# Kernel optimization log

Hardware: AMD Instinct MI355X
Metric: run time of the kernel (lower is better)

## Reference

```python
import jax, jax.numpy as jnp
import numpy as np

T, B, I = 2048, 256, 64
H = 1280          # hidden_size = 20 * input_size
H4 = H // 4       # fc2 out / LSTMCell input = 320
H8 = H // 8       # LSTMCell hidden = 160
O = 32            # output_size


def setup_inputs() -> dict:
    key = jax.random.key(0)
    ks = jax.random.split(key, 12)
    n = lambda k, shape, fan: jax.random.normal(k, shape, jnp.float32) * (1.0 / np.sqrt(fan))
    return {
        "inputs": jax.random.normal(ks[0], (T, B, I), jnp.float32),
        "W1": n(ks[1], (H, I), I),
        "b1": jnp.zeros((H,), jnp.float32),
        "W2": n(ks[2], (H4, H), H),
        "b2": jnp.zeros((H4,), jnp.float32),
        "W_ih": n(ks[3], (4 * H8, H4), H4),
        "W_hh": n(ks[4], (4 * H8, H8), H8),
        "b_ih": jnp.zeros((4 * H8,), jnp.float32),
        "b_hh": jnp.zeros((4 * H8,), jnp.float32),
        "W3": n(ks[5], (O, H8), H8),
        "b3": jnp.zeros((O,), jnp.float32),
    }


def reference(inputs, W1, b1, W2, b2, W_ih, W_hh, b_ih, b_hh, W3, b3):
    # Eval-mode forward: dropout / noise are identity when not training.
    Bd = inputs.shape[1]
    Hc = W_hh.shape[1]

    def step(carry, x_t):
        h, c = carry
        x = jax.nn.leaky_relu(x_t @ W1.T + b1)          # [B, H]
        x = jax.nn.leaky_relu(x @ W2.T + b2)            # [B, H//4]
        gates = x @ W_ih.T + b_ih + h @ W_hh.T + b_hh   # [B, 4*H//8]
        i, f, g, o = jnp.split(gates, 4, axis=-1)       # PyTorch gate order i,f,g,o
        i = jax.nn.sigmoid(i)
        f = jax.nn.sigmoid(f)
        g = jnp.tanh(g)
        o = jax.nn.sigmoid(o)
        c = f * c + i * g
        h = o * jnp.tanh(c)
        y = h @ W3.T + b3                                # [B, O]
        return (h, c), y

    h0 = jnp.zeros((Bd, Hc), inputs.dtype)
    c0 = jnp.zeros((Bd, Hc), inputs.dtype)
    _, ys = jax.lax.scan(step, (h0, c0), inputs)         # [T, B, O]
    return ys
```

## Files before the change

### kernel.cpp

```cpp
#include <hip/hip_runtime.h>
#include <hip/hip_bf16.h>

#define T_STEPS 2048
#define BATCH   256
#define INW     64
#define H1      1280
#define H4D     320
#define H8D     160
#define G4      640
#define ONUM    32

typedef __attribute__((ext_vector_type(8))) short short8;
typedef __attribute__((ext_vector_type(4))) float floatx4;
typedef __hip_bfloat16 bf16;

__device__ __forceinline__ float b2f(bf16 v) { return __bfloat162float(v); }
__device__ __forceinline__ bf16  f2b(float v) { return __float2bfloat16(v); }
__device__ __forceinline__ float bfu(unsigned short u) { return __uint_as_float((unsigned)u << 16); }
__device__ __forceinline__ float fsig(float x)  { return __fdividef(1.0f, 1.0f + __expf(-x)); }
__device__ __forceinline__ float ftanh(float x) { return __fdividef(2.0f, 1.0f + __expf(-2.0f * x)) - 1.0f; }

__device__ __forceinline__ void lds_barrier() {
  asm volatile("s_waitcnt lgkmcnt(0)\n\ts_barrier" ::: "memory");
}

struct bf16x4 { bf16 a, b, c, d; };
__global__ void cast_f32_bf16_v4(const float* __restrict__ s, bf16* __restrict__ d, int n4) {
  int i = blockIdx.x * blockDim.x + threadIdx.x;
  if (i >= n4) return;
  float4 v = reinterpret_cast<const float4*>(s)[i];
  bf16x4 o{f2b(v.x), f2b(v.y), f2b(v.z), f2b(v.w)};
  reinterpret_cast<bf16x4*>(d)[i] = o;
}

#define SMEM_BYTES 41472

__device__ void gemm_tile(char* smem, int tid, int mt, int nt,
                          const bf16* __restrict__ A, const bf16* __restrict__ W,
                          const float* __restrict__ bias, const float* __restrict__ bias2,
                          bf16* __restrict__ C, int N, int K, int ACT)
{
  bf16 (*As)[72] = reinterpret_cast<bf16 (*)[72]>(smem);
  bf16 (*Ws)[72] = reinterpret_cast<bf16 (*)[72]>(smem + 128 * 72 * 2);
  const int lane = tid & 63;
  const int wave = tid >> 6;
  const int mrow = lane & 15;
  const int quad = lane >> 4;
  const int wm = (wave >= 5) ? 64 : 0;
  const int wn = (wave - (wave >= 5 ? 5 : 0)) * 32;
  const int bm = mt * 128;
  const int bn = nt * 160;

  floatx4 acc[4][2] = {};

  const int va0 = tid, va1 = tid + 640;
  const int vw0 = tid, vw1 = tid + 640;

  for (int k0 = 0; k0 < K; k0 += 64) {
    short8 a0, a1, w0, w1;
    a0 = *reinterpret_cast<const short8*>(&A[(size_t)(bm + (va0 >> 3)) * K + k0 + (va0 & 7) * 8]);
    if (va1 < 1024)
      a1 = *reinterpret_cast<const short8*>(&A[(size_t)(bm + (va1 >> 3)) * K + k0 + (va1 & 7) * 8]);
    w0 = *reinterpret_cast<const short8*>(&W[(size_t)(bn + (vw0 >> 3)) * K + k0 + (vw0 & 7) * 8]);
    w1 = *reinterpret_cast<const short8*>(&W[(size_t)(bn + (vw1 >> 3)) * K + k0 + (vw1 & 7) * 8]);
    __syncthreads();
    *reinterpret_cast<short8*>(&As[va0 >> 3][(va0 & 7) * 8]) = a0;
    if (va1 < 1024)
      *reinterpret_cast<short8*>(&As[va1 >> 3][(va1 & 7) * 8]) = a1;
    *reinterpret_cast<short8*>(&Ws[vw0 >> 3][(vw0 & 7) * 8]) = w0;
    *reinterpret_cast<short8*>(&Ws[vw1 >> 3][(vw1 & 7) * 8]) = w1;
    __syncthreads();
#pragma unroll
    for (int kk = 0; kk < 2; ++kk) {
      short8 af[4], wf[2];
#pragma unroll
      for (int i = 0; i < 4; ++i)
        af[i] = *reinterpret_cast<const short8*>(&As[wm + i * 16 + mrow][kk * 32 + quad * 8]);
#pragma unroll
      for (int j = 0; j < 2; ++j)
        wf[j] = *reinterpret_cast<const short8*>(&Ws[wn + j * 16 + mrow][kk * 32 + quad * 8]);
#pragma unroll
      for (int i = 0; i < 4; ++i)
#pragma unroll
        for (int j = 0; j < 2; ++j)
          acc[i][j] = __builtin_amdgcn_mfma_f32_16x16x32_bf16(af[i], wf[j], acc[i][j], 0, 0, 0);
    }
  }

#pragma unroll
  for (int j = 0; j < 2; ++j) {
    int col = bn + wn + j * 16 + mrow;
    float bv = (ACT == 2) ? (bias[col] + bias2[col]) : bias[col];
    int g = 0, ix = 0;
    if (ACT == 2) { g = col / 160; ix = col - g * 160; }
#pragma unroll
    for (int i = 0; i < 4; ++i) {
#pragma unroll
      for (int r = 0; r < 4; ++r) {
        int row = bm + wm + i * 16 + quad * 4 + r;
        float v = acc[i][j][r] + bv;
        if (ACT == 1) {
          v = (v > 0.0f) ? v : 0.01f * v;
          C[(size_t)row * N + col] = f2b(v);
        } else {
          C[(size_t)row * 640 + ix * 4 + g] = f2b(v);
        }
      }
    }
  }
}

__device__ void recur_path(char* smem, int tid, int bid,
    const bf16* __restrict__ gx, const bf16* __restrict__ Whh,
    const bf16* __restrict__ W3w, const float* __restrict__ b3,
    bf16* __restrict__ h_ws, float* __restrict__ c_ws,
    float* __restrict__ outp, int Tc, int init)
{
  bf16 (*hbuf)[16][168] = reinterpret_cast<bf16 (*)[16][168]>(smem);
  bf16 (*w3s)[168] = reinterpret_cast<bf16 (*)[168]>(smem + 10752);
  const int lane = tid & 63;
  const int wave = tid >> 6;
  const int mrow = lane & 15;
  const int quad = lane >> 4;
  const int bbase = bid * 4;
  const int ixg = wave * 16 + mrow;

  short8 whf[4][5];
#pragma unroll
  for (int g = 0; g < 4; ++g)
#pragma unroll
    for (int ks = 0; ks < 5; ++ks)
      whf[g][ks] = *reinterpret_cast<const short8*>(
          &Whh[(size_t)(g * 160 + ixg) * 160 + ks * 32 + quad * 8]);

  for (int e = tid; e < 32 * 160; e += 640) {
    int r = e / 160, cix = e - r * 160;
    w3s[r][cix] = W3w[e];
  }
  const float b3v = (wave < 2) ? b3[wave * 16 + mrow] : 0.0f;

  for (int e = tid; e < 2 * 16 * 168; e += 640)
    reinterpret_cast<bf16*>(hbuf)[e] = f2b(0.0f);
  __syncthreads();
  {
    int r = tid / 160, cix = tid - r * 160;
    hbuf[0][r * 4][cix] = init ? f2b(0.0f) : h_ws[(size_t)(bbase + r) * 160 + cix];
  }
  float c0 = init ? 0.0f : c_ws[(size_t)(bbase + quad) * 160 + ixg];
  __syncthreads();

  const uint2* __restrict__ gxp = reinterpret_cast<const uint2*>(gx);
  const size_t goff = (size_t)(bbase + quad) * 160 + ixg;
  uint2 gcur = gxp[goff], gnext = gcur;

  for (int t = 0; t < Tc; ++t) {
    const int rb = t & 1, wb = rb ^ 1;
    if (t + 1 < Tc) gnext = gxp[(size_t)(t + 1) * (256 * 160) + goff];

    short8 af[5];
#pragma unroll
    for (int ks = 0; ks < 5; ++ks)
      af[ks] = *reinterpret_cast<const short8*>(&hbuf[rb][mrow][ks * 32 + quad * 8]);

    if (wave < 2 && t > 0) {
      short8 w3f[5];
#pragma unroll
      for (int ks = 0; ks < 5; ++ks)
        w3f[ks] = *reinterpret_cast<const short8*>(&w3s[wave * 16 + mrow][ks * 32 + quad * 8]);
      floatx4 ya = {};
#pragma unroll
      for (int ks = 0; ks < 5; ++ks)
        ya = __builtin_amdgcn_mfma_f32_16x16x32_bf16(af[ks], w3f[ks], ya, 0, 0, 0);
      outp[((size_t)(t - 1) * 256 + bbase + quad) * 32 + wave * 16 + mrow] = ya[0] + b3v;
    }

    floatx4 acc[4] = {};
#pragma unroll
    for (int ks = 0; ks < 5; ++ks)
#pragma unroll
      for (int g = 0; g < 4; ++g)
        acc[g] = __builtin_amdgcn_mfma_f32_16x16x32_bf16(af[ks], whf[g][ks], acc[g], 0, 0, 0);

    {
      union { uint2 u; unsigned short s[4]; } q;
      q.u = gcur;
      float xi = acc[0][0] + bfu(q.s[0]);
      float xf = acc[1][0] + bfu(q.s[1]);
      float xg = acc[2][0] + bfu(q.s[2]);
      float xo = acc[3][0] + bfu(q.s[3]);
      float iv = fsig(xi), fv = fsig(xf), gvv = ftanh(xg), ov = fsig(xo);
      c0 = fv * c0 + iv * gvv;
      hbuf[wb][quad * 4][ixg] = f2b(ov * ftanh(c0));
    }
    gcur = gnext;
    lds_barrier();
  }

  if (wave < 2) {
    const int rb = Tc & 1;
    short8 af[5], w3f[5];
#pragma unroll
    for (int ks = 0; ks < 5; ++ks) {
      af[ks]  = *reinterpret_cast<const short8*>(&hbuf[rb][mrow][ks * 32 + quad * 8]);
      w3f[ks] = *reinterpret_cast<const short8*>(&w3s[wave * 16 + mrow][ks * 32 + quad * 8]);
    }
    floatx4 ya = {};
#pragma unroll
    for (int ks = 0; ks < 5; ++ks)
      ya = __builtin_amdgcn_mfma_f32_16x16x32_bf16(af[ks], w3f[ks], ya, 0, 0, 0);
    outp[((size_t)(Tc - 1) * 256 + bbase + quad) * 32 + wave * 16 + mrow] = ya[0] + b3v;
  }

  {
    int r = tid / 160, cix = tid - r * 160;
    h_ws[(size_t)(bbase + r) * 160 + cix] = hbuf[Tc & 1][r * 4][cix];
  }
  c_ws[(size_t)(bbase + quad) * 160 + ixg] = c0;
}

__global__ __launch_bounds__(640, 1) void fused_step(
    int has_recur, const bf16* gxr, const bf16* Whh, const bf16* W3w,
    const float* b3, bf16* h_ws, float* c_ws, float* outp, int Tc, int init,
    int nb1, const bf16* A1, const bf16* W1w, const float* b1v, bf16* C1,
    int nb2, const bf16* A2, const bf16* W2w, const float* b2v, bf16* C2,
    int nb3, const bf16* A3, const bf16* Wiw, const float* bihv, const float* bhhv, bf16* C3,
    int nM)
{
  __shared__ __align__(16) char smem[SMEM_BYTES];
  const int tid = threadIdx.x;
  if (blockIdx.x < 64) {
    if (has_recur)
      recur_path(smem, tid, blockIdx.x, gxr, Whh, W3w, b3, h_ws, c_ws, outp, Tc, init);
    return;
  }
  int gb = blockIdx.x - 64;
  if (gb < nb1) {
    gemm_tile(smem, tid, gb % nM, gb / nM, A1, W1w, b1v, nullptr, C1, H1, INW, 1);
    return;
  }
  gb -= nb1;
  if (gb < nb2) {
    gemm_tile(smem, tid, gb % nM, gb / nM, A2, W2w, b2v, nullptr, C2, H4D, H1, 1);
    return;
  }
  gb -= nb2;
  gemm_tile(smem, tid, gb % nM, gb / nM, A3, Wiw, bihv, bhhv, C3, G4, H4D, 2);
}

extern "C" void kernel_launch(void* const* d_in, const int* in_sizes, int n_in,
                              void* d_out, int out_size, void* d_ws, size_t ws_size,
                              hipStream_t stream)
{
  const float* inp = (const float*)d_in[0];
  const float* W1  = (const float*)d_in[1];
  const float* b1  = (const float*)d_in[2];
  const float* W2  = (const float*)d_in[3];
  const float* b2  = (const float*)d_in[4];
  const float* Wih = (const float*)d_in[5];
  const float* Whh = (const float*)d_in[6];
  const float* bih = (const float*)d_in[7];
  const float* bhh = (const float*)d_in[8];
  const float* W3  = (const float*)d_in[9];
  const float* b3  = (const float*)d_in[10];
  float* out = (float*)d_out;

  char* ws = (char*)d_ws;
  size_t off = 0;
  auto alloc = [&](size_t bytes) -> char* {
    char* p = ws + off;
    off += (bytes + 255) & ~(size_t)255;
    return p;
  };

  bf16* inpb = (bf16*)alloc((size_t)T_STEPS * BATCH * INW * 2);
  bf16* w1b  = (bf16*)alloc((size_t)H1 * INW * 2);
  bf16* w2b  = (bf16*)alloc((size_t)H4D * H1 * 2);
  bf16* wihb = (bf16*)alloc((size_t)G4 * H4D * 2);
  bf16* whhb = (bf16*)alloc((size_t)G4 * H8D * 2);
  bf16* w3b  = (bf16*)alloc((size_t)ONUM * H8D * 2);
  bf16* h_ws = (bf16*)alloc((size_t)BATCH * H8D * 2);
  float* c_ws = (float*)alloc((size_t)BATCH * H8D * 4);
  size_t fixed = off;

  int Tc = 128;
  while (Tc > 16) {
    size_t Mc = (size_t)Tc * BATCH;
    size_t need = fixed
      + 2 * ((Mc * H1 * 2 + 255) & ~(size_t)255)
      + 2 * ((Mc * H4D * 2 + 255) & ~(size_t)255)
      + 2 * ((Mc * G4 * 2 + 255) & ~(size_t)255);
    if (need <= ws_size) break;
    Tc >>= 1;
  }
  const size_t Mc = (size_t)Tc * BATCH;
  bf16* x2b[2], *x4b[2], *gxb[2];
  for (int i = 0; i < 2; ++i) x2b[i] = (bf16*)alloc(Mc * H1 * 2);
  for (int i = 0; i < 2; ++i) x4b[i] = (bf16*)alloc(Mc * H4D * 2);
  for (int i = 0; i < 2; ++i) gxb[i] = (bf16*)alloc(Mc * G4 * 2);

  {
    int n4 = T_STEPS * BATCH * INW / 4;
    cast_f32_bf16_v4<<<(n4 + 255) / 256, 256, 0, stream>>>(inp, inpb, n4);
    n4 = H1 * INW / 4;
    cast_f32_bf16_v4<<<(n4 + 255) / 256, 256, 0, stream>>>(W1, w1b, n4);
    n4 = H4D * H1 / 4;
    cast_f32_bf16_v4<<<(n4 + 255) / 256, 256, 0, stream>>>(W2, w2b, n4);
    n4 = G4 * H4D / 4;
    cast_f32_bf16_v4<<<(n4 + 255) / 256, 256, 0, stream>>>(Wih, wihb, n4);
    n4 = G4 * H8D / 4;
    cast_f32_bf16_v4<<<(n4 + 255) / 256, 256, 0, stream>>>(Whh, whhb, n4);
    n4 = ONUM * H8D / 4;
    cast_f32_bf16_v4<<<(n4 + 255) / 256, 256, 0, stream>>>(W3, w3b, n4);
  }

  const int nch = T_STEPS / Tc;
  const int nM = (int)(Mc / 128);

  for (int L = 0; L < nch + 3; ++L) {
    const int cr = L - 3, c1 = L, c2 = L - 1, c3 = L - 2;
    const int nb1 = (c1 >= 0 && c1 < nch) ? nM * (H1 / 160) : 0;
    const int nb2 = (c2 >= 0 && c2 < nch) ? nM * (H4D / 160) : 0;
    const int nb3 = (c3 >= 0 && c3 < nch) ? nM * (G4 / 160) : 0;
    const int hasr = (cr >= 0 && cr < nch) ? 1 : 0;

    const bf16* gxr = gxb[hasr ? (cr & 1) : 0];
    float* outp = hasr ? (out + (size_t)cr * Tc * BATCH * ONUM) : out;
    const bf16* A1 = nb1 ? (inpb + (size_t)c1 * Mc * INW) : inpb;
    bf16* C1 = x2b[nb1 ? (c1 & 1) : 0];
    const bf16* A2 = x2b[nb2 ? (c2 & 1) : 0];
    bf16* C2 = x4b[nb2 ? (c2 & 1) : 0];
    const bf16* A3 = x4b[nb3 ? (c3 & 1) : 0];
    bf16* C3 = gxb[nb3 ? (c3 & 1) : 0];

    fused_step<<<64 + nb1 + nb2 + nb3, 640, 0, stream>>>(
        hasr, gxr, whhb, w3b, b3, h_ws, c_ws, outp, Tc, (cr == 0) ? 1 : 0,
        nb1, A1, w1b, b1, C1,
        nb2, A2, w2b, b2, C2,
        nb3, A3, wihb, bih, bhh, C3,
        nM);
  }
}
```

Before: 2.973 ms.

## Fuse fc1, fc2 and LSTM input projection into one per-tile GEMM chain

```diff
diff --git a/kernel.cpp b/kernel.cpp
--- a/kernel.cpp
+++ b/kernel.cpp
@@ -14,6 +14,8 @@
 typedef __attribute__((ext_vector_type(4))) float floatx4;
 typedef __hip_bfloat16 bf16;
 
+union frag8 { short8 v; uint2 u2[2]; };
+
 __device__ __forceinline__ float b2f(bf16 v) { return __bfloat162float(v); }
 __device__ __forceinline__ bf16  f2b(float v) { return __float2bfloat16(v); }
 __device__ __forceinline__ float bfu(unsigned short u) { return __uint_as_float((unsigned)u << 16); }
@@ -33,78 +35,203 @@
   reinterpret_cast<bf16x4*>(d)[i] = o;
 }
 
-#define SMEM_BYTES 41472
-
-__device__ void gemm_tile(char* smem, int tid, int mt, int nt,
-                          const bf16* __restrict__ A, const bf16* __restrict__ W,
-                          const float* __restrict__ bias, const float* __restrict__ bias2,
-                          bf16* __restrict__ C, int N, int K, int ACT)
+__global__ void cast_permute_wih(const float* __restrict__ s, bf16* __restrict__ d) {
+  int i = blockIdx.x * blockDim.x + threadIdx.x;
+  if (i >= G4 * (H4D / 4)) return;
+  int p = i / (H4D / 4), k4 = (i - p * (H4D / 4)) * 4;
+  int g = p & 3, ix = p >> 2;
+  float4 v = *reinterpret_cast<const float4*>(&s[(size_t)(g * 160 + ix) * H4D + k4]);
+  bf16x4 o{f2b(v.x), f2b(v.y), f2b(v.z), f2b(v.w)};
+  *reinterpret_cast<bf16x4*>(&d[(size_t)p * H4D + k4]) = o;
+}
+
+#define SMEM_BYTES 65024
+
+__device__ void fused_gemm(char* smem, int tid, int gb,
+    const bf16* __restrict__ Xg, const bf16* __restrict__ W1g, const float* __restrict__ b1v,
+    const bf16* __restrict__ W2g, const float* __restrict__ b2v,
+    const bf16* __restrict__ Wpg, const float* __restrict__ bihv, const float* __restrict__ bhhv,
+    bf16* __restrict__ gxw)
 {
-  bf16 (*As)[72] = reinterpret_cast<bf16 (*)[72]>(smem);
-  bf16 (*Ws)[72] = reinterpret_cast<bf16 (*)[72]>(smem + 128 * 72 * 2);
-  const int lane = tid & 63;
-  const int wave = tid >> 6;
-  const int mrow = lane & 15;
-  const int quad = lane >> 4;
-  const int wm = (wave >= 5) ? 64 : 0;
-  const int wn = (wave - (wave >= 5 ? 5 : 0)) * 32;
-  const int bm = mt * 128;
-  const int bn = nt * 160;
-
-  floatx4 acc[4][2] = {};
-
-  const int va0 = tid, va1 = tid + 640;
-  const int vw0 = tid, vw1 = tid + 640;
-
-  for (int k0 = 0; k0 < K; k0 += 64) {
-    short8 a0, a1, w0, w1;
-    a0 = *reinterpret_cast<const short8*>(&A[(size_t)(bm + (va0 >> 3)) * K + k0 + (va0 & 7) * 8]);
-    if (va1 < 1024)
-      a1 = *reinterpret_cast<const short8*>(&A[(size_t)(bm + (va1 >> 3)) * K + k0 + (va1 & 7) * 8]);
-    w0 = *reinterpret_cast<const short8*>(&W[(size_t)(bn + (vw0 >> 3)) * K + k0 + (vw0 & 7) * 8]);
-    w1 = *reinterpret_cast<const short8*>(&W[(size_t)(bn + (vw1 >> 3)) * K + k0 + (vw1 & 7) * 8]);
-    __syncthreads();
-    *reinterpret_cast<short8*>(&As[va0 >> 3][(va0 & 7) * 8]) = a0;
-    if (va1 < 1024)
-      *reinterpret_cast<short8*>(&As[va1 >> 3][(va1 & 7) * 8]) = a1;
-    *reinterpret_cast<short8*>(&Ws[vw0 >> 3][(vw0 & 7) * 8]) = w0;
-    *reinterpret_cast<short8*>(&Ws[vw1 >> 3][(vw1 & 7) * 8]) = w1;
-    __syncthreads();
+  bf16 (*Y1s)[72]  = reinterpret_cast<bf16 (*)[72]>(smem);
+  bf16 (*W2cs)[72] = reinterpret_cast<bf16 (*)[72]>(smem + 9216);
+  const int lane = tid & 63, wave = tid >> 6;
+  const int mrow = lane & 15, quad = lane >> 4;
+  const int wm = (wave >= 5) ? 1 : 0;
+  const int wn = wave - wm * 5;
+  const int fm = wave & 3;
+  const int fnp = (wave >> 2) & 1;
+  const size_t R0 = (size_t)gb * 64;
+
+  short8 xf0, xf1;
+  if (wave < 8) {
+    const bf16* xrow = Xg + (R0 + fm * 16 + mrow) * INW;
+    xf0 = *reinterpret_cast<const short8*>(xrow + quad * 8);
+    xf1 = *reinterpret_cast<const short8*>(xrow + 32 + quad * 8);
+  }
+
+  short8 w2r[4];
+#pragma unroll
+  for (int i = 0; i < 4; ++i) {
+    int v = tid + i * 640;
+    w2r[i] = *reinterpret_cast<const short8*>(&W2g[(size_t)(v >> 3) * H1 + (v & 7) * 8]);
+  }
+#pragma unroll
+  for (int i = 0; i < 4; ++i) {
+    int v = tid + i * 640;
+    *reinterpret_cast<short8*>(&W2cs[v >> 3][(v & 7) * 8]) = w2r[i];
+  }
+
+  floatx4 acc2[2][4] = {};
+
+  for (int c = 0; c < 20; ++c) {
+    if (wave < 8) {
+      const bf16* wr0 = W1g + (size_t)(c * 64 + (fnp * 2 + 0) * 16 + mrow) * INW;
+      const bf16* wr1 = W1g + (size_t)(c * 64 + (fnp * 2 + 1) * 16 + mrow) * INW;
+      short8 wf00 = *reinterpret_cast<const short8*>(wr0 + quad * 8);
+      short8 wf01 = *reinterpret_cast<const short8*>(wr0 + 32 + quad * 8);
+      short8 wf10 = *reinterpret_cast<const short8*>(wr1 + quad * 8);
+      short8 wf11 = *reinterpret_cast<const short8*>(wr1 + 32 + quad * 8);
+      floatx4 a10 = {}, a11 = {};
+      a10 = __builtin_amdgcn_mfma_f32_16x16x32_bf16(xf0, wf00, a10, 0, 0, 0);
+      a10 = __builtin_amdgcn_mfma_f32_16x16x32_bf16(xf1, wf01, a10, 0, 0, 0);
+      a11 = __builtin_amdgcn_mfma_f32_16x16x32_bf16(xf0, wf10, a11, 0, 0, 0);
+      a11 = __builtin_amdgcn_mfma_f32_16x16x32_bf16(xf1, wf11, a11, 0, 0, 0);
+#pragma unroll
+      for (int r = 0; r < 4; ++r) {
+        int row = fm * 16 + quad * 4 + r;
+        {
+          int col = (fnp * 2 + 0) * 16 + mrow;
+          float vv = a10[r] + b1v[c * 64 + col];
+          Y1s[row][col] = f2b(vv > 0.0f ? vv : 0.01f * vv);
+        }
+        {
+          int col = (fnp * 2 + 1) * 16 + mrow;
+          float vv = a11[r] + b1v[c * 64 + col];
+          Y1s[row][col] = f2b(vv > 0.0f ? vv : 0.01f * vv);
+        }
+      }
+    }
+    if (c < 19) {
+#pragma unroll
+      for (int i = 0; i < 4; ++i) {
+        int v = tid + i * 640;
+        w2r[i] = *reinterpret_cast<const short8*>(
+            &W2g[(size_t)(v >> 3) * H1 + (c + 1) * 64 + (v & 7) * 8]);
+      }
+    }
+    lds_barrier();
 #pragma unroll
     for (int kk = 0; kk < 2; ++kk) {
-      short8 af[4], wf[2];
-#pragma unroll
-      for (int i = 0; i < 4; ++i)
-        af[i] = *reinterpret_cast<const short8*>(&As[wm + i * 16 + mrow][kk * 32 + quad * 8]);
-#pragma unroll
-      for (int j = 0; j < 2; ++j)
-        wf[j] = *reinterpret_cast<const short8*>(&Ws[wn + j * 16 + mrow][kk * 32 + quad * 8]);
-#pragma unroll
-      for (int i = 0; i < 4; ++i)
-#pragma unroll
-        for (int j = 0; j < 2; ++j)
-          acc[i][j] = __builtin_amdgcn_mfma_f32_16x16x32_bf16(af[i], wf[j], acc[i][j], 0, 0, 0);
-    }
-  }
-
-#pragma unroll
-  for (int j = 0; j < 2; ++j) {
-    int col = bn + wn + j * 16 + mrow;
-    float bv = (ACT == 2) ? (bias[col] + bias2[col]) : bias[col];
-    int g = 0, ix = 0;
-    if (ACT == 2) { g = col / 160; ix = col - g * 160; }
-#pragma unroll
-    for (int i = 0; i < 4; ++i) {
+      short8 af0 = *reinterpret_cast<const short8*>(&Y1s[wm * 32 + mrow][kk * 32 + quad * 8]);
+      short8 af1 = *reinterpret_cast<const short8*>(&Y1s[wm * 32 + 16 + mrow][kk * 32 + quad * 8]);
+#pragma unroll
+      for (int j = 0; j < 4; ++j) {
+        short8 bfj = *reinterpret_cast<const short8*>(
+            &W2cs[wn * 64 + j * 16 + mrow][kk * 32 + quad * 8]);
+        acc2[0][j] = __builtin_amdgcn_mfma_f32_16x16x32_bf16(af0, bfj, acc2[0][j], 0, 0, 0);
+        acc2[1][j] = __builtin_amdgcn_mfma_f32_16x16x32_bf16(af1, bfj, acc2[1][j], 0, 0, 0);
+      }
+    }
+    lds_barrier();
+    if (c < 19) {
+#pragma unroll
+      for (int i = 0; i < 4; ++i) {
+        int v = tid + i * 640;
+        *reinterpret_cast<short8*>(&W2cs[v >> 3][(v & 7) * 8]) = w2r[i];
+      }
+    }
+  }
+
+  bf16 (*Y2s)[328] = reinterpret_cast<bf16 (*)[328]>(smem);
+  char* Wps = smem + 41984;
+  short8 wpr[2];
+#pragma unroll
+  for (int i = 0; i < 2; ++i) {
+    int v = tid + i * 640;
+    wpr[i] = *reinterpret_cast<const short8*>(&Wpg[(size_t)(v >> 2) * H4D + (v & 3) * 8]);
+  }
+#pragma unroll
+  for (int i = 0; i < 2; ++i) {
+#pragma unroll
+    for (int j = 0; j < 4; ++j) {
+      int col = wn * 64 + j * 16 + mrow;
+      float bb = b2v[col];
 #pragma unroll
       for (int r = 0; r < 4; ++r) {
-        int row = bm + wm + i * 16 + quad * 4 + r;
-        float v = acc[i][j][r] + bv;
-        if (ACT == 1) {
-          v = (v > 0.0f) ? v : 0.01f * v;
-          C[(size_t)row * N + col] = f2b(v);
-        } else {
-          C[(size_t)row * 640 + ix * 4 + g] = f2b(v);
-        }
+        int row = wm * 32 + i * 16 + quad * 4 + r;
+        float vv = acc2[i][j][r] + bb;
+        Y2s[row][col] = f2b(vv > 0.0f ? vv : 0.01f * vv);
+      }
+    }
+  }
+#pragma unroll
+  for (int i = 0; i < 2; ++i) {
+    int v = tid + i * 640;
+    frag8 u; u.v = wpr[i];
+    char* p = Wps + (size_t)(v >> 2) * 72 + (v & 3) * 16;
+    *reinterpret_cast<uint2*>(p) = u.u2[0];
+    *reinterpret_cast<uint2*>(p + 8) = u.u2[1];
+  }
+  lds_barrier();
+
+  floatx4 ag[2][4];
+  for (int t = 0; t < 20; ++t) {
+    int h = t / 10, kc = t - h * 10;
+    if (kc == 0) {
+#pragma unroll
+      for (int i = 0; i < 2; ++i)
+#pragma unroll
+        for (int j = 0; j < 4; ++j) ag[i][j] = (floatx4){0.f, 0.f, 0.f, 0.f};
+    }
+    short8 af0 = *reinterpret_cast<const short8*>(&Y2s[wm * 32 + mrow][kc * 32 + quad * 8]);
+    short8 af1 = *reinterpret_cast<const short8*>(&Y2s[wm * 32 + 16 + mrow][kc * 32 + quad * 8]);
+    frag8 bfj[4];
+#pragma unroll
+    for (int j = 0; j < 4; ++j) {
+      const char* p = Wps + (size_t)(wn * 64 + j * 16 + mrow) * 72 + quad * 16;
+      bfj[j].u2[0] = *reinterpret_cast<const uint2*>(p);
+      bfj[j].u2[1] = *reinterpret_cast<const uint2*>(p + 8);
+    }
+#pragma unroll
+    for (int j = 0; j < 4; ++j) {
+      ag[0][j] = __builtin_amdgcn_mfma_f32_16x16x32_bf16(af0, bfj[j].v, ag[0][j], 0, 0, 0);
+      ag[1][j] = __builtin_amdgcn_mfma_f32_16x16x32_bf16(af1, bfj[j].v, ag[1][j], 0, 0, 0);
+    }
+    if (t < 19) {
+      int nh = (t + 1) / 10, nk = (t + 1) - nh * 10;
+#pragma unroll
+      for (int i = 0; i < 2; ++i) {
+        int v = tid + i * 640;
+        wpr[i] = *reinterpret_cast<const short8*>(
+            &Wpg[(size_t)(nh * 320 + (v >> 2)) * H4D + nk * 32 + (v & 3) * 8]);
+      }
+    }
+    lds_barrier();
+    if (t < 19) {
+#pragma unroll
+      for (int i = 0; i < 2; ++i) {
+        int v = tid + i * 640;
+        frag8 u; u.v = wpr[i];
+        char* p = Wps + (size_t)(v >> 2) * 72 + (v & 3) * 16;
+        *reinterpret_cast<uint2*>(p) = u.u2[0];
+        *reinterpret_cast<uint2*>(p + 8) = u.u2[1];
+      }
+    }
+    lds_barrier();
+    if (kc == 9) {
+#pragma unroll
+      for (int j = 0; j < 4; ++j) {
+        int p = h * 320 + wn * 64 + j * 16 + mrow;
+        int g = p & 3, ix = p >> 2;
+        float bb = bihv[g * 160 + ix] + bhhv[g * 160 + ix];
+#pragma unroll
+        for (int i = 0; i < 2; ++i)
+#pragma unroll
+          for (int r = 0; r < 4; ++r) {
+            int row = wm * 32 + i * 16 + quad * 4 + r;
+            gxw[(R0 + row) * 640 + p] = f2b(ag[i][j][r] + bb);
+          }
       }
     }
   }
@@ -218,13 +345,12 @@
   c_ws[(size_t)(bbase + quad) * 160 + ixg] = c0;
 }
 
-__global__ __launch_bounds__(640, 1) void fused_step(
+__global__ __launch_bounds__(640, 5) void fused_step(
     int has_recur, const bf16* gxr, const bf16* Whh, const bf16* W3w,
     const float* b3, bf16* h_ws, float* c_ws, float* outp, int Tc, int init,
-    int nb1, const bf16* A1, const bf16* W1w, const float* b1v, bf16* C1,
-    int nb2, const bf16* A2, const bf16* W2w, const float* b2v, bf16* C2,
-    int nb3, const bf16* A3, const bf16* Wiw, const float* bihv, const float* bhhv, bf16* C3,
-    int nM)
+    int has_gemm, const bf16* Xc, const bf16* W1w, const float* b1v,
+    const bf16* W2w, const float* b2v, const bf16* Wpw,
+    const float* bihv, const float* bhhv, bf16* gxw)
 {
   __shared__ __align__(16) char smem[SMEM_BYTES];
   const int tid = threadIdx.x;
@@ -233,18 +359,8 @@
       recur_path(smem, tid, blockIdx.x, gxr, Whh, W3w, b3, h_ws, c_ws, outp, Tc, init);
     return;
   }
-  int gb = blockIdx.x - 64;
-  if (gb < nb1) {
-    gemm_tile(smem, tid, gb % nM, gb / nM, A1, W1w, b1v, nullptr, C1, H1, INW, 1);
-    return;
-  }
-  gb -= nb1;
-  if (gb < nb2) {
-    gemm_tile(smem, tid, gb % nM, gb / nM, A2, W2w, b2v, nullptr, C2, H4D, H1, 1);
-    return;
-  }
-  gb -= nb2;
-  gemm_tile(smem, tid, gb % nM, gb / nM, A3, Wiw, bihv, bhhv, C3, G4, H4D, 2);
+  if (has_gemm)
+    fused_gemm(smem, tid, blockIdx.x - 64, Xc, W1w, b1v, W2w, b2v, Wpw, bihv, bhhv, gxw);
 }
 
 extern "C" void kernel_launch(void* const* d_in, const int* in_sizes, int n_in,
@@ -275,7 +391,7 @@
   bf16* inpb = (bf16*)alloc((size_t)T_STEPS * BATCH * INW * 2);
   bf16* w1b  = (bf16*)alloc((size_t)H1 * INW * 2);
   bf16* w2b  = (bf16*)alloc((size_t)H4D * H1 * 2);
-  bf16* wihb = (bf16*)alloc((size_t)G4 * H4D * 2);
+  bf16* wpb  = (bf16*)alloc((size_t)G4 * H4D * 2);
   bf16* whhb = (bf16*)alloc((size_t)G4 * H8D * 2);
   bf16* w3b  = (bf16*)alloc((size_t)ONUM * H8D * 2);
   bf16* h_ws = (bf16*)alloc((size_t)BATCH * H8D * 2);
@@ -285,17 +401,12 @@
   int Tc = 128;
   while (Tc > 16) {
     size_t Mc = (size_t)Tc * BATCH;
-    size_t need = fixed
-      + 2 * ((Mc * H1 * 2 + 255) & ~(size_t)255)
-      + 2 * ((Mc * H4D * 2 + 255) & ~(size_t)255)
-      + 2 * ((Mc * G4 * 2 + 255) & ~(size_t)255);
+    size_t need = fixed + 2 * ((Mc * G4 * 2 + 255) & ~(size_t)255);
     if (need <= ws_size) break;
     Tc >>= 1;
   }
   const size_t Mc = (size_t)Tc * BATCH;
-  bf16* x2b[2], *x4b[2], *gxb[2];
-  for (int i = 0; i < 2; ++i) x2b[i] = (bf16*)alloc(Mc * H1 * 2);
-  for (int i = 0; i < 2; ++i) x4b[i] = (bf16*)alloc(Mc * H4D * 2);
+  bf16* gxb[2];
   for (int i = 0; i < 2; ++i) gxb[i] = (bf16*)alloc(Mc * G4 * 2);
 
   {
@@ -305,8 +416,8 @@
     cast_f32_bf16_v4<<<(n4 + 255) / 256, 256, 0, stream>>>(W1, w1b, n4);
     n4 = H4D * H1 / 4;
     cast_f32_bf16_v4<<<(n4 + 255) / 256, 256, 0, stream>>>(W2, w2b, n4);
-    n4 = G4 * H4D / 4;
-    cast_f32_bf16_v4<<<(n4 + 255) / 256, 256, 0, stream>>>(Wih, wihb, n4);
+    int np = G4 * (H4D / 4);
+    cast_permute_wih<<<(np + 255) / 256, 256, 0, stream>>>(Wih, wpb);
     n4 = G4 * H8D / 4;
     cast_f32_bf16_v4<<<(n4 + 255) / 256, 256, 0, stream>>>(Whh, whhb, n4);
     n4 = ONUM * H8D / 4;
@@ -314,29 +425,18 @@
   }
 
   const int nch = T_STEPS / Tc;
-  const int nM = (int)(Mc / 128);
-
-  for (int L = 0; L < nch + 3; ++L) {
-    const int cr = L - 3, c1 = L, c2 = L - 1, c3 = L - 2;
-    const int nb1 = (c1 >= 0 && c1 < nch) ? nM * (H1 / 160) : 0;
-    const int nb2 = (c2 >= 0 && c2 < nch) ? nM * (H4D / 160) : 0;
-    const int nb3 = (c3 >= 0 && c3 < nch) ? nM * (G4 / 160) : 0;
-    const int hasr = (cr >= 0 && cr < nch) ? 1 : 0;
-
-    const bf16* gxr = gxb[hasr ? (cr & 1) : 0];
-    float* outp = hasr ? (out + (size_t)cr * Tc * BATCH * ONUM) : out;
-    const bf16* A1 = nb1 ? (inpb + (size_t)c1 * Mc * INW) : inpb;
-    bf16* C1 = x2b[nb1 ? (c1 & 1) : 0];
-    const bf16* A2 = x2b[nb2 ? (c2 & 1) : 0];
-    bf16* C2 = x4b[nb2 ? (c2 & 1) : 0];
-    const bf16* A3 = x4b[nb3 ? (c3 & 1) : 0];
-    bf16* C3 = gxb[nb3 ? (c3 & 1) : 0];
-
-    fused_step<<<64 + nb1 + nb2 + nb3, 640, 0, stream>>>(
-        hasr, gxr, whhb, w3b, b3, h_ws, c_ws, outp, Tc, (cr == 0) ? 1 : 0,
-        nb1, A1, w1b, b1, C1,
-        nb2, A2, w2b, b2, C2,
-        nb3, A3, wihb, bih, bhh, C3,
-        nM);
-  }
-}
+  const int nGB = (int)(Mc / 64);
+
+  for (int L = 0; L <= nch; ++L) {
+    const int hg = (L < nch) ? 1 : 0;
+    const int hr = (L >= 1) ? 1 : 0;
+    const bf16* Xc = inpb + (size_t)(hg ? L : 0) * Mc * INW;
+    bf16* gxw = gxb[L & 1];
+    const bf16* gxr = gxb[(L + 1) & 1];
+    float* outp = hr ? (out + (size_t)(L - 1) * Tc * BATCH * ONUM) : out;
+
+    fused_step<<<64 + (hg ? nGB : 0), 640, 0, stream>>>(
+        hr, gxr, whhb, w3b, b3, h_ws, c_ws, outp, Tc, (L == 1) ? 1 : 0,
+        hg, Xc, w1b, b1, w2b, b2, wpb, bih, bhh, gxw);
+  }
+}
```

New measurement: 7.061 ms. +137.5%, slower.
